# Kernel tuning notes

Measured on AMD Instinct MI355X. Metric: run time of the kernel, lower is better.

The kernel has to match this reference:

```python
import jax, jax.numpy as jnp
import numpy as np

HEADS = 16
HEAD_DIM = 32
WINDOW = 64  # kernel_size = 2*WINDOW + 1 = 129
NEG = -1e30


def setup_inputs() -> dict:
    key = jax.random.key(0)
    ks = jax.random.split(key, 9)
    B, T, D, G = 4, 8192, HEADS * HEAD_DIM, 64
    x = jax.random.normal(ks[0], (B, T, D), jnp.float32)
    def W(k):
        return jax.random.normal(k, (D, D), jnp.float32) * 0.02
    def b(k):
        return jax.random.normal(k, (D,), jnp.float32) * 0.02
    return {
        "x": x,
        "Wq": W(ks[1]), "bq": b(ks[2]),
        "Wk": W(ks[3]), "bk": b(ks[4]),
        "Wv": W(ks[5]), "bv": b(ks[6]),
        "Wo": W(ks[7]), "bo": b(ks[8]),
        "global_idx": jnp.arange(G, dtype=jnp.int64 if jax.config.jax_enable_x64 else jnp.int32),
    }


def _sparse_global_attn(x, Wq, bq, Wk, bk, Wv, bv, Wo, bo, global_idx):
    B, T, D = x.shape
    H, d, w = HEADS, HEAD_DIM, WINDOW
    scale = 1.0 / (d ** 0.5)

    def proj(W, b):
        # (B,T,D) -> (B,H,T,d)
        return (x @ W + b).reshape(B, T, H, d).transpose(0, 2, 1, 3)

    q, k, v = proj(Wq, bq), proj(Wk, bk), proj(Wv, bv)

    offsets = jnp.arange(-w, w + 1)  # (K,)
    K = offsets.shape[0]

    # Local band scores: score[b,h,t,j] = <q[t], k[t+offset_j]>, computed
    # offset-by-offset via roll to avoid a (B,H,T,K,d) gather.
    def score_step(_, o):
        s = jnp.einsum('bhtd,bhtd->bht', q, jnp.roll(k, -o, axis=2))
        return None, s
    _, loc = jax.lax.scan(score_step, None, offsets)  # (K,B,H,T)
    loc = jnp.moveaxis(loc, 0, -1) * scale            # (B,H,T,K)

    pos = jnp.arange(T)[:, None] + offsets[None, :]   # (T,K)
    valid = (pos >= 0) & (pos < T)
    loc = jnp.where(valid[None, None], loc, NEG)

    # Global-token scores (global tokens shared across the batch)
    k_g = k[:, :, global_idx, :]                      # (B,H,G,d)
    v_g = v[:, :, global_idx, :]
    gsc = jnp.einsum('bhtd,bhgd->bhtg', q, k_g) * scale  # (B,H,T,G)

    # Joint softmax over [local window | global tokens] (duplicates where a
    # global token lies inside the local window, matching the original).
    attn = jax.nn.softmax(jnp.concatenate([loc, gsc], axis=-1), axis=-1)
    a_loc = jnp.moveaxis(attn[..., :K], -1, 0)        # (K,B,H,T)
    a_g = attn[..., K:]                               # (B,H,T,G)

    def ctx_step(acc, oa):
        o, a = oa
        return acc + a[..., None] * jnp.roll(v, -o, axis=2), None
    ctx, _ = jax.lax.scan(ctx_step, jnp.zeros_like(q), (offsets, a_loc))
    ctx = ctx + jnp.einsum('bhtg,bhgd->bhtd', a_g, v_g)  # (B,H,T,d)

    out = ctx.transpose(0, 2, 1, 3).reshape(B, T, D)
    return out @ Wo + bo


def reference(x, Wq, bq, Wk, bk, Wv, bv, Wo, bo, global_idx):
    return _sparse_global_attn(x, Wq, bq, Wk, bk, Wv, bv, Wo, bo, global_idx)
```

## Files before the change

### kernel.cpp

```cpp
#include <hip/hip_runtime.h>
#include <hip/hip_bf16.h>
#include <cstdint>
#include <cstddef>

using bf16 = __hip_bfloat16;
typedef __bf16 bf16x8 __attribute__((ext_vector_type(8)));
typedef float f32x4 __attribute__((ext_vector_type(4)));

constexpr int BB = 4;
constexpr int TS = 8192;
constexpr int NH = 16;
constexpr int HD = 32;
constexpr int DM = 512;
constexpr int NQKV = 1536;
constexpr int NG = 64;

#define MFMA16(a, b, c) __builtin_amdgcn_mfma_f32_16x16x32_bf16((a), (b), (c), 0, 0, 0)

__device__ __forceinline__ bf16x8 ld8(const bf16* p) { return *(const bf16x8*)p; }
__device__ __forceinline__ unsigned short b16bits(bf16 v) { return __builtin_bit_cast(unsigned short, v); }

__device__ __forceinline__ void gl_lds16(const bf16* g, void* l) {
  __builtin_amdgcn_global_load_lds((const __attribute__((address_space(1))) void*)g,
                                   (__attribute__((address_space(3))) void*)l, 16, 0, 0);
}

__global__ void prep_kernel(const float* __restrict__ x,
                            const float* __restrict__ Wq, const float* __restrict__ bq,
                            const float* __restrict__ Wk, const float* __restrict__ bk,
                            const float* __restrict__ Wv, const float* __restrict__ bv,
                            const float* __restrict__ Wo,
                            bf16* __restrict__ xb, bf16* __restrict__ Wt,
                            bf16* __restrict__ Wot, float* __restrict__ bqkv) {
  const int64_t stride = (int64_t)gridDim.x * blockDim.x;
  const int64_t i0 = (int64_t)blockIdx.x * blockDim.x + threadIdx.x;
  const float4* x4 = (const float4*)x;
  ushort4* xb4 = (ushort4*)xb;
  for (int64_t i = i0; i < (int64_t)BB * TS * DM / 4; i += stride) {
    float4 v = x4[i];
    ushort4 o;
    o.x = b16bits(__float2bfloat16(v.x));
    o.y = b16bits(__float2bfloat16(v.y));
    o.z = b16bits(__float2bfloat16(v.z));
    o.w = b16bits(__float2bfloat16(v.w));
    xb4[i] = o;
  }
  for (int64_t i = i0; i < (int64_t)NQKV * DM; i += stride) {
    const int n = (int)(i >> 9), k = (int)(i & 511);
    const float* W = (n < 512) ? Wq : ((n < 1024) ? Wk : Wv);
    Wt[i] = __float2bfloat16(W[(size_t)k * DM + (n & 511)]);
  }
  for (int64_t i = i0; i < (int64_t)DM * DM; i += stride) {
    const int n = (int)(i >> 9), k = (int)(i & 511);
    Wot[i] = __float2bfloat16(Wo[(size_t)k * DM + n]);
  }
  for (int64_t i = i0; i < NQKV; i += stride)
    bqkv[i] = (i < 512) ? bq[i] : ((i < 1024) ? bk[i - 512] : bv[i - 1024]);
}

template <bool F32OUT, bool WVT>
__global__ __launch_bounds__(256) void gemm_bias(const bf16* __restrict__ A,
                                                 const bf16* __restrict__ Bt,
                                                 const float* __restrict__ bias,
                                                 void* __restrict__ Cv,
                                                 bf16* __restrict__ vt,
                                                 int M, int N, int K, int cpx) {
  __shared__ __attribute__((aligned(16))) char smem[65536];
  const int tid = threadIdx.x;
  const int lane = tid & 63, wid = tid >> 6;
  const int grp = lane >> 4, col = lane & 15;
  const int bid = (blockIdx.x & 7) * cpx + (blockIdx.x >> 3);
  const int NT = N >> 7;
  const int mt = bid / NT, nt = bid % NT;
  const int m0 = mt << 7, n0 = nt << 7;
  const int wm = wid >> 1, wn = wid & 1;
  f32x4 acc[4][4] = {};
  const int KT = K >> 6;

  auto stage = [&](int kt, int d) {
    #pragma unroll
    for (int c = 0; c < 4; ++c) {
      const int chunk = wid * 4 + c;
      const int row = chunk * 8 + (lane >> 3);
      const int sl = lane & 7;
      const int koff = ((sl ^ (row & 7)) << 3) + (kt << 6);
      gl_lds16(A + (size_t)(m0 + row) * K + koff, smem + d * 16384 + chunk * 1024);
      gl_lds16(Bt + (size_t)(n0 + row) * K + koff,
               smem + 32768 + d * 16384 + chunk * 1024);
    }
  };

  stage(0, 0);
  for (int kt = 0; kt < KT; ++kt) {
    const int cur = kt & 1;
    if (kt + 1 < KT) {
      stage(kt + 1, cur ^ 1);
      __builtin_amdgcn_sched_barrier(0);
      asm volatile("s_waitcnt vmcnt(8)" ::: "memory");
    } else {
      __builtin_amdgcn_sched_barrier(0);
      asm volatile("s_waitcnt vmcnt(0)" ::: "memory");
    }
    __builtin_amdgcn_sched_barrier(0);
    __builtin_amdgcn_s_barrier();
    __builtin_amdgcn_sched_barrier(0);
    const char* sA = smem + cur * 16384;
    const char* sB = smem + 32768 + cur * 16384;
    #pragma unroll
    for (int ks = 0; ks < 2; ++ks) {
      bf16x8 af[4], bfr[4];
      #pragma unroll
      for (int f = 0; f < 4; ++f) {
        const int ra = wm * 64 + f * 16 + col;
        af[f] = *(const bf16x8*)(sA + ra * 128 + (((ks * 4 + grp) ^ (ra & 7)) << 4));
        const int rb = wn * 64 + f * 16 + col;
        bfr[f] = *(const bf16x8*)(sB + rb * 128 + (((ks * 4 + grp) ^ (rb & 7)) << 4));
      }
      #pragma unroll
      for (int i = 0; i < 4; ++i)
        #pragma unroll
        for (int j = 0; j < 4; ++j)
          acc[i][j] = MFMA16(af[i], bfr[j], acc[i][j]);
    }
    __builtin_amdgcn_sched_barrier(0);
    __builtin_amdgcn_s_barrier();
    __builtin_amdgcn_sched_barrier(0);
  }
  const bool wv = WVT && (n0 >= 1024);
  if (!wv) {
    #pragma unroll
    for (int i = 0; i < 4; ++i)
      #pragma unroll
      for (int j = 0; j < 4; ++j) {
        const int n = n0 + wn * 64 + j * 16 + col;
        const float bz = bias[n];
        #pragma unroll
        for (int r = 0; r < 4; ++r) {
          const int m = m0 + wm * 64 + i * 16 + grp * 4 + r;
          const float v = acc[i][j][r] + bz;
          if (F32OUT)
            ((float*)Cv)[(size_t)m * N + n] = v;
          else
            ((bf16*)Cv)[(size_t)m * N + n] = __float2bfloat16(v);
        }
      }
  } else {
    __syncthreads();
    bf16* lt = (bf16*)smem;
    #pragma unroll
    for (int i = 0; i < 4; ++i)
      #pragma unroll
      for (int j = 0; j < 4; ++j) {
        const int nl = wn * 64 + j * 16 + col;
        const float bz = bias[n0 + nl];
        #pragma unroll
        for (int r = 0; r < 4; ++r) {
          const int ml = wm * 64 + i * 16 + grp * 4 + r;
          lt[nl * 136 + (ml ^ ((nl & 7) << 4))] = __float2bfloat16(acc[i][j][r] + bz);
        }
      }
    __syncthreads();
    const int row = tid >> 1, half = tid & 1;
    const int b = m0 >> 13, t0 = m0 & 8191;
    bf16* dst = vt + (size_t)(b * DM + (n0 & 511) + row) * TS + t0 + half * 64;
    const bf16* srcl = lt + row * 136;
    #pragma unroll
    for (int c = 0; c < 8; ++c)
      *(bf16x8*)(dst + c * 8) =
          *(const bf16x8*)(srcl + ((half * 64 + c * 8) ^ ((row & 7) << 4)));
  }
}

__global__ void vgt_kernel(const bf16* __restrict__ vt, const int* __restrict__ gidx,
                           bf16* __restrict__ vtp, bf16* __restrict__ vgt) {
  const int64_t stride = (int64_t)gridDim.x * blockDim.x;
  const int64_t i0 = (int64_t)blockIdx.x * blockDim.x + threadIdx.x;
  for (int64_t i = i0; i < 512; i += stride) {
    if (i < 64) vtp[i - 64] = __float2bfloat16(0.f);
    else vtp[(size_t)2048 * TS + (i - 64)] = __float2bfloat16(0.f);
  }
  for (int64_t i = i0; i < (int64_t)2048 * NG; i += stride) {
    const int row = (int)(i >> 6), g = (int)(i & 63);
    const int gi = gidx[g];
    vgt[i] = vt[(size_t)row * TS + gi];
  }
}

__global__ __launch_bounds__(256) void attn_kernel(const bf16* __restrict__ qkv,
                                                   const bf16* __restrict__ vt,
                                                   const bf16* __restrict__ vgt,
                                                   const int* __restrict__ gidx,
                                                   bf16* __restrict__ ctx) {
  constexpr int PROW = 240;
  constexpr int VST = 216;
  constexpr int VGST = 88;
  __shared__ __attribute__((aligned(16))) char smem[50176];
  bf16* sV = (bf16*)smem;
  bf16* sVg = (bf16*)(smem + 13824);
  bf16* sK = (bf16*)(smem + 19456);
  bf16* sKg = (bf16*)(smem + 31744);
  bf16* sP = (bf16*)(smem + 19456);

  const int tid = threadIdx.x, wid = tid >> 6, lane = tid & 63;
  const int grp = lane >> 4, col = lane & 15;
  const int bid = (blockIdx.x & 7) * 1024 + (blockIdx.x >> 3);
  const int tile = bid & 127, h = (bid >> 7) & 15, b = bid >> 11;
  const int t0b = tile * 64;
  const int kbb = t0b - 64;
  const int bh = b * NH + h;
  const bf16* base = qkv + (size_t)b * TS * NQKV;
  const bf16* kpl = base + 512 + h * 32;

  #pragma unroll
  for (int it = 0; it < 3; ++it) {
    const int idx = it * 256 + tid;
    const int row = idx >> 2, part = idx & 3;
    const int tok = min(max(kbb + row, 0), TS - 1);
    gl_lds16(kpl + (size_t)tok * NQKV + ((part ^ (row & 3)) << 3), sK + idx * 8);
  }
  {
    const int row = tid >> 2, part = tid & 3;
    const int gi = gidx[row];
    gl_lds16(kpl + (size_t)gi * NQKV + ((part ^ (row & 3)) << 3), sKg + tid * 8);
  }
  {
    const bf16* vr = vt + (size_t)(bh * HD + (tid >> 3)) * TS + kbb;
    #pragma unroll
    for (int i = 0; i < 4; ++i) {
      const int c = i * 8 + (tid & 7);
      if (c < 27) *(bf16x8*)(sV + (tid >> 3) * VST + c * 8) = ld8(vr + c * 8);
    }
  }
  {
    const int row = tid >> 3, c = tid & 7;
    *(bf16x8*)(sVg + row * VGST + c * 8) = ld8(vgt + (size_t)(bh * HD + row) * NG + c * 8);
  }
  __syncthreads();

  const int qt = t0b + wid * 16;
  const int offw = wid * 16;
  bf16* myP = sP + wid * 16 * PROW;

  const bf16x8 qf = ld8(base + (size_t)(qt + col) * NQKV + h * 32 + grp * 8);
  const f32x4 z = {0.f, 0.f, 0.f, 0.f};
  f32x4 s[13];
  #pragma unroll
  for (int f = 0; f < 9; ++f) {
    const int row = offw + f * 16 + col;
    bf16x8 kf = ld8(sK + row * 32 + ((grp ^ (row & 3)) << 3));
    s[f] = MFMA16(qf, kf, z);
  }
  #pragma unroll
  for (int f = 0; f < 4; ++f) {
    const int row = f * 16 + col;
    bf16x8 kf = ld8(sKg + row * 32 + ((grp ^ (row & 3)) << 3));
    s[9 + f] = MFMA16(qf, kf, z);
  }
  const float scale = 0.17677669529663688f;
  float mx[4] = {-3e38f, -3e38f, -3e38f, -3e38f};
  const bool interior = (tile >= 1) & (tile <= 126);
  if (interior) {
    #pragma unroll
    for (int f = 0; f < 13; ++f) {
      #pragma unroll
      for (int r = 0; r < 4; ++r) {
        float v = s[f][r] * scale;
        if (f == 0) v = (col >= grp * 4 + r) ? v : -1e30f;
        if (f == 8) v = (col <= grp * 4 + r) ? v : -1e30f;
        s[f][r] = v;
        mx[r] = fmaxf(mx[r], v);
      }
    }
  } else {
    #pragma unroll
    for (int f = 0; f < 13; ++f) {
      #pragma unroll
      for (int r = 0; r < 4; ++r) {
        float v = s[f][r] * scale;
        if (f < 9) {
          const int q = grp * 4 + r;
          const int j = f * 16 + col;
          const int pos = qt - 64 + j;
          const bool valid = (j >= q) & (j <= q + 128) & (pos >= 0) & (pos < TS);
          v = valid ? v : -1e30f;
        }
        s[f][r] = v;
        mx[r] = fmaxf(mx[r], v);
      }
    }
  }
  #pragma unroll
  for (int r = 0; r < 4; ++r) {
    #pragma unroll
    for (int d = 1; d < 16; d <<= 1) mx[r] = fmaxf(mx[r], __shfl_xor(mx[r], d));
  }
  float sm[4] = {0.f, 0.f, 0.f, 0.f};
  #pragma unroll
  for (int f = 0; f < 13; ++f) {
    #pragma unroll
    for (int r = 0; r < 4; ++r) {
      float p = __expf(s[f][r] - mx[r]);
      s[f][r] = p;
      sm[r] += p;
    }
  }
  #pragma unroll
  for (int r = 0; r < 4; ++r) {
    #pragma unroll
    for (int d = 1; d < 16; d <<= 1) sm[r] += __shfl_xor(sm[r], d);
    sm[r] = 1.0f / sm[r];
  }
  __syncthreads();

  #pragma unroll
  for (int f = 0; f < 13; ++f) {
    const int j = f * 16 + col + ((f >= 9) ? 16 : 0);
    #pragma unroll
    for (int r = 0; r < 4; ++r)
      myP[(grp * 4 + r) * PROW + j] = __float2bfloat16(s[f][r]);
  }
  #pragma unroll
  for (int r = 0; r < 4; ++r)
    myP[(grp * 4 + r) * PROW + 144 + col] = __float2bfloat16(0.f);
  __threadfence_block();

  f32x4 c0 = z, c1 = z;
  #pragma unroll
  for (int ks = 0; ks < 5; ++ks) {
    bf16x8 pa = ld8(myP + col * PROW + ks * 32 + grp * 8);
    const int kk = offw + ks * 32 + grp * 8;
    bf16x8 v0 = ld8(sV + col * VST + kk);
    bf16x8 v1 = ld8(sV + (col + 16) * VST + kk);
    c0 = MFMA16(pa, v0, c0);
    c1 = MFMA16(pa, v1, c1);
  }
  #pragma unroll
  for (int ks = 0; ks < 2; ++ks) {
    bf16x8 pa = ld8(myP + col * PROW + 160 + ks * 32 + grp * 8);
    bf16x8 v0 = ld8(sVg + col * VGST + ks * 32 + grp * 8);
    bf16x8 v1 = ld8(sVg + (col + 16) * VGST + ks * 32 + grp * 8);
    c0 = MFMA16(pa, v0, c0);
    c1 = MFMA16(pa, v1, c1);
  }
  #pragma unroll
  for (int r = 0; r < 4; ++r) {
    const int t = qt + grp * 4 + r;
    const size_t o = ((size_t)(b * TS + t)) * DM + h * 32;
    ctx[o + col] = __float2bfloat16(c0[r] * sm[r]);
    ctx[o + 16 + col] = __float2bfloat16(c1[r] * sm[r]);
  }
}

extern "C" void kernel_launch(void* const* d_in, const int* in_sizes, int n_in,
                              void* d_out, int out_size, void* d_ws, size_t ws_size,
                              hipStream_t stream) {
  (void)in_sizes; (void)n_in; (void)out_size; (void)ws_size;
  const float* x = (const float*)d_in[0];
  const float* Wq = (const float*)d_in[1];
  const float* bq = (const float*)d_in[2];
  const float* Wk = (const float*)d_in[3];
  const float* bk = (const float*)d_in[4];
  const float* Wv = (const float*)d_in[5];
  const float* bv = (const float*)d_in[6];
  const float* Wo = (const float*)d_in[7];
  const float* bo = (const float*)d_in[8];
  const int* gidx = (const int*)d_in[9];
  float* out = (float*)d_out;

  char* ws = (char*)d_ws;
  size_t off = 0;
  auto alloc = [&](size_t bytes) -> void* {
    void* p = ws + off;
    off += (bytes + 255) & ~(size_t)255;
    return p;
  };
  bf16* xb = (bf16*)alloc((size_t)BB * TS * DM * 2);
  bf16* Wt = (bf16*)alloc((size_t)NQKV * DM * 2);
  bf16* Wot = (bf16*)alloc((size_t)DM * DM * 2);
  float* bqkv = (float*)alloc((size_t)NQKV * 4);
  bf16* qkv = (bf16*)alloc((size_t)BB * TS * NQKV * 2);
  bf16* vta = (bf16*)alloc(((size_t)2048 * TS + 512) * 2);
  bf16* vgt = (bf16*)alloc((size_t)2048 * NG * 2);
  bf16* ctx = xb;
  bf16* vt = vta + 64;

  prep_kernel<<<dim3(2048), dim3(256), 0, stream>>>(x, Wq, bq, Wk, bk, Wv, bv, Wo,
                                                    xb, Wt, Wot, bqkv);
  gemm_bias<false, true><<<dim3(3072), dim3(256), 0, stream>>>(xb, Wt, bqkv, qkv, vt,
                                                               BB * TS, NQKV, DM, 384);
  vgt_kernel<<<dim3(512), dim3(256), 0, stream>>>(vt, gidx, vt, vgt);
  attn_kernel<<<dim3(8192), dim3(256), 0, stream>>>(qkv, vt, vgt, gidx, ctx);
  gemm_bias<true, false><<<dim3(1024), dim3(256), 0, stream>>>(ctx, Wot, bo, out, nullptr,
                                                               BB * TS, DM, DM, 128);
}
```

Measured before the change: 195.5 us.

## Transpose QK MFMA so probabilities stay in registers as PV operand

Swaps the operand order of the score MFMA so each lane holds scores for one query across keys. The probabilities can then be packed directly into bf16 B-operands for the PV MFMA, with V loaded as the A operand. This drops the LDS round-trip for the P matrix, the second __syncthreads, and the 16-lane shuffle reductions, which become two xor shuffles. It also shrinks shared memory, which may raise occupancy, and vectorizes the context store. The cost is split 4-element V loads from LDS and the risk of index-mapping errors in the masking.

```diff
diff --git a/kernel.cpp b/kernel.cpp
--- a/kernel.cpp
+++ b/kernel.cpp
@@ -5,6 +5,7 @@
 
 using bf16 = __hip_bfloat16;
 typedef __bf16 bf16x8 __attribute__((ext_vector_type(8)));
+typedef __bf16 bf16x4 __attribute__((ext_vector_type(4)));
 typedef float f32x4 __attribute__((ext_vector_type(4)));
 
 constexpr int BB = 4;
@@ -18,6 +19,7 @@
 #define MFMA16(a, b, c) __builtin_amdgcn_mfma_f32_16x16x32_bf16((a), (b), (c), 0, 0, 0)
 
 __device__ __forceinline__ bf16x8 ld8(const bf16* p) { return *(const bf16x8*)p; }
+__device__ __forceinline__ bf16x4 ld4(const bf16* p) { return *(const bf16x4*)p; }
 __device__ __forceinline__ unsigned short b16bits(bf16 v) { return __builtin_bit_cast(unsigned short, v); }
 
 __device__ __forceinline__ void gl_lds16(const bf16* g, void* l) {
@@ -191,15 +193,13 @@
                                                    const bf16* __restrict__ vgt,
                                                    const int* __restrict__ gidx,
                                                    bf16* __restrict__ ctx) {
-  constexpr int PROW = 240;
   constexpr int VST = 216;
   constexpr int VGST = 88;
-  __shared__ __attribute__((aligned(16))) char smem[50176];
+  __shared__ __attribute__((aligned(16))) char smem[35840];
   bf16* sV = (bf16*)smem;
   bf16* sVg = (bf16*)(smem + 13824);
   bf16* sK = (bf16*)(smem + 19456);
   bf16* sKg = (bf16*)(smem + 31744);
-  bf16* sP = (bf16*)(smem + 19456);
 
   const int tid = threadIdx.x, wid = tid >> 6, lane = tid & 63;
   const int grp = lane >> 4, col = lane & 15;
@@ -239,7 +239,6 @@
 
   const int qt = t0b + wid * 16;
   const int offw = wid * 16;
-  bf16* myP = sP + wid * 16 * PROW;
 
   const bf16x8 qf = ld8(base + (size_t)(qt + col) * NQKV + h * 32 + grp * 8);
   const f32x4 z = {0.f, 0.f, 0.f, 0.f};
@@ -248,16 +247,16 @@
   for (int f = 0; f < 9; ++f) {
     const int row = offw + f * 16 + col;
     bf16x8 kf = ld8(sK + row * 32 + ((grp ^ (row & 3)) << 3));
-    s[f] = MFMA16(qf, kf, z);
+    s[f] = MFMA16(kf, qf, z);
   }
   #pragma unroll
   for (int f = 0; f < 4; ++f) {
     const int row = f * 16 + col;
     bf16x8 kf = ld8(sKg + row * 32 + ((grp ^ (row & 3)) << 3));
-    s[9 + f] = MFMA16(qf, kf, z);
+    s[9 + f] = MFMA16(kf, qf, z);
   }
   const float scale = 0.17677669529663688f;
-  float mx[4] = {-3e38f, -3e38f, -3e38f, -3e38f};
+  float mx = -3e38f;
   const bool interior = (tile >= 1) & (tile <= 126);
   if (interior) {
     #pragma unroll
@@ -265,10 +264,10 @@
       #pragma unroll
       for (int r = 0; r < 4; ++r) {
         float v = s[f][r] * scale;
-        if (f == 0) v = (col >= grp * 4 + r) ? v : -1e30f;
-        if (f == 8) v = (col <= grp * 4 + r) ? v : -1e30f;
+        if (f == 0) v = (grp * 4 + r >= col) ? v : -1e30f;
+        if (f == 8) v = (grp * 4 + r <= col) ? v : -1e30f;
         s[f][r] = v;
-        mx[r] = fmaxf(mx[r], v);
+        mx = fmaxf(mx, v);
       }
     }
   } else {
@@ -278,77 +277,75 @@
       for (int r = 0; r < 4; ++r) {
         float v = s[f][r] * scale;
         if (f < 9) {
-          const int q = grp * 4 + r;
-          const int j = f * 16 + col;
+          const int j = f * 16 + grp * 4 + r;
           const int pos = qt - 64 + j;
-          const bool valid = (j >= q) & (j <= q + 128) & (pos >= 0) & (pos < TS);
+          const bool valid = (j >= col) & (j <= col + 128) & (pos >= 0) & (pos < TS);
           v = valid ? v : -1e30f;
         }
         s[f][r] = v;
-        mx[r] = fmaxf(mx[r], v);
-      }
-    }
-  }
-  #pragma unroll
-  for (int r = 0; r < 4; ++r) {
-    #pragma unroll
-    for (int d = 1; d < 16; d <<= 1) mx[r] = fmaxf(mx[r], __shfl_xor(mx[r], d));
-  }
-  float sm[4] = {0.f, 0.f, 0.f, 0.f};
+        mx = fmaxf(mx, v);
+      }
+    }
+  }
+  mx = fmaxf(mx, __shfl_xor(mx, 16));
+  mx = fmaxf(mx, __shfl_xor(mx, 32));
+  float sum = 0.f;
+  bf16x8 pb[7];
   #pragma unroll
   for (int f = 0; f < 13; ++f) {
+    const int pr = (f < 9) ? (f >> 1) : (5 + ((f - 9) >> 1));
+    const int hf = (f < 9) ? (f & 1) : ((f - 9) & 1);
     #pragma unroll
     for (int r = 0; r < 4; ++r) {
-      float p = __expf(s[f][r] - mx[r]);
-      s[f][r] = p;
-      sm[r] += p;
-    }
-  }
-  #pragma unroll
-  for (int r = 0; r < 4; ++r) {
-    #pragma unroll
-    for (int d = 1; d < 16; d <<= 1) sm[r] += __shfl_xor(sm[r], d);
-    sm[r] = 1.0f / sm[r];
-  }
-  __syncthreads();
-
-  #pragma unroll
-  for (int f = 0; f < 13; ++f) {
-    const int j = f * 16 + col + ((f >= 9) ? 16 : 0);
-    #pragma unroll
-    for (int r = 0; r < 4; ++r)
-      myP[(grp * 4 + r) * PROW + j] = __float2bfloat16(s[f][r]);
-  }
-  #pragma unroll
-  for (int r = 0; r < 4; ++r)
-    myP[(grp * 4 + r) * PROW + 144 + col] = __float2bfloat16(0.f);
-  __threadfence_block();
+      float p = __expf(s[f][r] - mx);
+      sum += p;
+      pb[pr][hf * 4 + r] = (__bf16)__float2bfloat16(p);
+    }
+  }
+  #pragma unroll
+  for (int r = 0; r < 4; ++r) pb[4][4 + r] = (__bf16)__float2bfloat16(0.f);
+  sum += __shfl_xor(sum, 16);
+  sum += __shfl_xor(sum, 32);
+  const float sm = 1.0f / sum;
 
   f32x4 c0 = z, c1 = z;
-  #pragma unroll
-  for (int ks = 0; ks < 5; ++ks) {
-    bf16x8 pa = ld8(myP + col * PROW + ks * 32 + grp * 8);
-    const int kk = offw + ks * 32 + grp * 8;
-    bf16x8 v0 = ld8(sV + col * VST + kk);
-    bf16x8 v1 = ld8(sV + (col + 16) * VST + kk);
-    c0 = MFMA16(pa, v0, c0);
-    c1 = MFMA16(pa, v1, c1);
-  }
-  #pragma unroll
-  for (int ks = 0; ks < 2; ++ks) {
-    bf16x8 pa = ld8(myP + col * PROW + 160 + ks * 32 + grp * 8);
-    bf16x8 v0 = ld8(sVg + col * VGST + ks * 32 + grp * 8);
-    bf16x8 v1 = ld8(sVg + (col + 16) * VGST + ks * 32 + grp * 8);
-    c0 = MFMA16(pa, v0, c0);
-    c1 = MFMA16(pa, v1, c1);
-  }
-  #pragma unroll
-  for (int r = 0; r < 4; ++r) {
-    const int t = qt + grp * 4 + r;
-    const size_t o = ((size_t)(b * TS + t)) * DM + h * 32;
-    ctx[o + col] = __float2bfloat16(c0[r] * sm[r]);
-    ctx[o + 16 + col] = __float2bfloat16(c1[r] * sm[r]);
-  }
+  const bf16* sVr0 = sV + col * VST;
+  const bf16* sVr1 = sV + (col + 16) * VST;
+  #pragma unroll
+  for (int i = 0; i < 5; ++i) {
+    const int kk = offw + i * 32 + grp * 4;
+    bf16x8 a0 = __builtin_shufflevector(ld4(sVr0 + kk), ld4(sVr0 + kk + 16),
+                                        0, 1, 2, 3, 4, 5, 6, 7);
+    bf16x8 a1 = __builtin_shufflevector(ld4(sVr1 + kk), ld4(sVr1 + kk + 16),
+                                        0, 1, 2, 3, 4, 5, 6, 7);
+    c0 = MFMA16(a0, pb[i], c0);
+    c1 = MFMA16(a1, pb[i], c1);
+  }
+  const bf16* sVg0 = sVg + col * VGST;
+  const bf16* sVg1 = sVg + (col + 16) * VGST;
+  #pragma unroll
+  for (int i = 0; i < 2; ++i) {
+    const int kk = i * 32 + grp * 4;
+    bf16x8 a0 = __builtin_shufflevector(ld4(sVg0 + kk), ld4(sVg0 + kk + 16),
+                                        0, 1, 2, 3, 4, 5, 6, 7);
+    bf16x8 a1 = __builtin_shufflevector(ld4(sVg1 + kk), ld4(sVg1 + kk + 16),
+                                        0, 1, 2, 3, 4, 5, 6, 7);
+    c0 = MFMA16(a0, pb[5 + i], c0);
+    c1 = MFMA16(a1, pb[5 + i], c1);
+  }
+  const int t = qt + col;
+  bf16* op = ctx + ((size_t)(b * TS + t)) * DM + h * 32 + grp * 4;
+  ushort4 o0, o1;
+  o0.x = b16bits(__float2bfloat16(c0[0] * sm));
+  o0.y = b16bits(__float2bfloat16(c0[1] * sm));
+  o0.z = b16bits(__float2bfloat16(c0[2] * sm));
+  o0.w = b16bits(__float2bfloat16(c0[3] * sm));
+  o1.x = b16bits(__float2bfloat16(c1[0] * sm));
+  o1.y = b16bits(__float2bfloat16(c1[1] * sm));
+  o1.z = b16bits(__float2bfloat16(c1[2] * sm));
+  o1.w = b16bits(__float2bfloat16(c1[3] * sm));
+  *(ushort4*)op = o0;
+  *(ushort4*)(op + 16) = o1;
 }
 
 extern "C" void kernel_launch(void* const* d_in, const int* in_sizes, int n_in,
```

Result: faster. 172.8 us (-11.6%).
